# Optimization experiments

Hardware: AMD Instinct MI355X
Metric: run time of the kernel (lower is better)

Reference implementation:

```python
import jax, jax.numpy as jnp
import numpy as np
import math

N, LQ, C, HD, L, P = 2, 17821, 256, 8, 4, 4
D = C // HD
SHAPES = [(100, 134), (50, 67), (25, 34), (13, 17)]


def setup_inputs() -> dict:
    key = jax.random.key(0)
    ks = jax.random.split(key, 8)
    shapes = np.array(SHAPES, np.int32)
    areas = shapes[:, 0] * shapes[:, 1]
    starts = np.concatenate([[0], np.cumsum(areas)[:-1]]).astype(np.int32)
    Lin = int(areas.sum())
    sc = 1.0 / math.sqrt(C)
    # sampling_offsets bias: radial grid init as in _reset_parameters
    thetas = np.arange(HD, dtype=np.float32) * (2.0 * math.pi / HD)
    grid = np.stack([np.cos(thetas), np.sin(thetas)], -1)
    grid = grid / np.abs(grid).max(-1, keepdims=True)
    grid = np.tile(grid[:, None, None, :], (1, L, P, 1)) * np.arange(1, P + 1, dtype=np.float32)[None, None, :, None]
    boff = jnp.asarray(grid.reshape(-1), jnp.float32)
    return dict(
        query=jax.random.normal(ks[0], (N, LQ, C), jnp.float32),
        reference_points=jax.random.uniform(ks[1], (N, LQ, L, 2), jnp.float32),
        input_flatten=jax.random.normal(ks[2], (N, Lin, C), jnp.float32),
        input_spatial_shapes=jnp.asarray(shapes),
        input_level_start_index=jnp.asarray(starts),
        Wv=jax.random.normal(ks[3], (C, C), jnp.float32) * sc,
        bv=jnp.zeros((C,), jnp.float32),
        Woff=jax.random.normal(ks[4], (C, HD * L * P * 2), jnp.float32) * 0.01,
        boff=boff,
        Watt=jax.random.normal(ks[5], (C, HD * L * P), jnp.float32) * 0.02,
        batt=jnp.zeros((HD * L * P,), jnp.float32),
        Wout=jax.random.normal(ks[6], (C, C), jnp.float32) * sc,
        bout=jnp.zeros((C,), jnp.float32),
    )


def _ms_deform_attn_core(value, shapes, starts, loc, attw):
    # value: (N, Len_in, HD, D); loc: (N, Lq, HD, L, P, 2) in [0,1]; attw: (N, Lq, HD, L, P)
    n, lq = loc.shape[0], loc.shape[1]
    out = jnp.zeros((n, lq, HD, D), value.dtype)
    for l in range(L):
        H, W = int(shapes[l, 0]), int(shapes[l, 1])
        s = int(starts[l])
        v = value[:, s:s + H * W]                                    # (N, HW, HD, D)
        # (N,Lq,HD,P,2) -> (N,Lq,P,HD,2) -> (N,Lq*P,HD) per coord
        locl = loc[:, :, :, l].transpose(0, 1, 3, 2, 4).reshape(n, lq * P, HD, 2)
        # grid_sample align_corners=False mapping
        x = locl[..., 0] * W - 0.5
        y = locl[..., 1] * H - 0.5
        x0f, y0f = jnp.floor(x), jnp.floor(y)
        fx, fy = x - x0f, y - y0f
        x0, y0 = x0f.astype(jnp.int32), y0f.astype(jnp.int32)

        def corner(xi, yi, w):
            valid = (xi >= 0) & (xi < W) & (yi >= 0) & (yi < H)      # zero padding
            idx = jnp.clip(yi, 0, H - 1) * W + jnp.clip(xi, 0, W - 1)
            g = jnp.take_along_axis(v, idx[..., None], axis=1)        # (N, Lq*P, HD, D)
            return g * (w * valid)[..., None]

        samp = (corner(x0, y0, (1 - fx) * (1 - fy))
                + corner(x0 + 1, y0, fx * (1 - fy))
                + corner(x0, y0 + 1, (1 - fx) * fy)
                + corner(x0 + 1, y0 + 1, fx * fy))                    # (N, Lq*P, HD, D)
        aw = attw[:, :, :, l].transpose(0, 1, 3, 2).reshape(n, lq * P, HD)
        out = out + (samp * aw[..., None]).reshape(n, lq, P, HD, D).sum(axis=2)
    return out.reshape(n, lq, HD * D)


def reference(query, reference_points, input_flatten, input_spatial_shapes,
              input_level_start_index, Wv, bv, Woff, boff, Watt, batt, Wout, bout):
    shapes = np.asarray(input_spatial_shapes)
    starts = np.asarray(input_level_start_index)
    n, lq, _ = query.shape
    value = (input_flatten @ Wv + bv).reshape(n, -1, HD, D)
    offsets = (query @ Woff + boff).reshape(n, lq, HD, L, P, 2)
    # reference_points has last dim 2 -> normalize offsets by (W, H) per level
    norm = jnp.asarray(shapes[:, ::-1], jnp.float32)                  # (L, 2) = (W, H)
    loc = reference_points[:, :, None, :, None, :] + offsets / norm[None, None, None, :, None, :]
    attw = (query @ Watt + batt).reshape(n, lq, HD, L * P)
    attw = jax.nn.softmax(attw, axis=-1).reshape(n, lq, HD, L, P)
    out = _ms_deform_attn_core(value, shapes, starts, loc, attw)
    return out @ Wout + bout
```

## Files before the change

### kernel.cpp

```cpp
#include <hip/hip_runtime.h>
#include <hip/hip_bf16.h>
#include <math.h>

#define NB    2
#define LQ    17821
#define LIN   17821
#define CCH   256
#define HDN   8
#define DCH   32
#define LVL   4
#define NPT   4
#define KDIM  256

__constant__ const int   cH[LVL]  = {100, 50, 25, 13};
__constant__ const int   cW[LVL]  = {134, 67, 34, 17};
__constant__ const int   cS[LVL]  = {0, 13400, 16750, 17600};
__constant__ const float cHf[LVL] = {100.f, 50.f, 25.f, 13.f};
__constant__ const float cWf[LVL] = {134.f, 67.f, 34.f, 17.f};
__constant__ const float cRH[LVL] = {1.f/100.f, 1.f/50.f, 1.f/25.f, 1.f/13.f};
__constant__ const float cRW[LVL] = {1.f/134.f, 1.f/67.f, 1.f/34.f, 1.f/17.f};

typedef __attribute__((ext_vector_type(8))) _Float16 f16x8;
typedef __attribute__((ext_vector_type(4))) _Float16 f16x4;
typedef __attribute__((ext_vector_type(4))) float    f32x4;

__device__ __forceinline__ void glds16(const void* g, void* l) {
    __builtin_amdgcn_global_load_lds(
        (const __attribute__((address_space(1))) void*)g,
        (__attribute__((address_space(3))) void*)l, 16, 0, 0);
}

__global__ void prep_all(const float* __restrict__ Wv,
                         const float* __restrict__ Woff,
                         const float* __restrict__ Watt,
                         const float* __restrict__ Wout,
                         const float* __restrict__ boff,
                         const float* __restrict__ batt,
                         _Float16* __restrict__ wvT,
                         _Float16* __restrict__ wqT,
                         _Float16* __restrict__ wuT,
                         float* __restrict__ b384)
{
    const int i = blockIdx.x * 256 + threadIdx.x;
    if (i < 65536) {
        const int n = i >> 8, k = i & 255;
        wvT[i] = (_Float16)Wv[(size_t)k * 256 + n];
    } else if (i < 131072) {
        const int j = i - 65536, n = j >> 8, k = j & 255;
        wqT[j] = (_Float16)Woff[(size_t)k * 256 + n];
    } else if (i < 163840) {
        const int j = i - 131072, n = j >> 8, k = j & 255;
        wqT[65536 + j] = (_Float16)Watt[(size_t)k * 128 + n];
    } else if (i < 229376) {
        const int j = i - 163840, n = j >> 8, k = j & 255;
        wuT[j] = (_Float16)Wout[(size_t)k * 256 + n];
    } else {
        const int j = i - 229376;
        if (j < 256)      b384[j] = boff[j];
        else if (j < 384) b384[j] = batt[j - 256];
    }
}

__global__ void cvt_two(const float* __restrict__ X0, const float* __restrict__ X1,
                        _Float16* __restrict__ Y0, _Float16* __restrict__ Y1, int n4)
{
    const int stride = gridDim.x * 256;
    for (int i = blockIdx.x * 256 + threadIdx.x; i < 2 * n4; i += stride) {
        const bool second = i >= n4;
        const int j = second ? i - n4 : i;
        const float4 v = reinterpret_cast<const float4*>(second ? X1 : X0)[j];
        f16x4 h;
        h[0] = (_Float16)v.x; h[1] = (_Float16)v.y;
        h[2] = (_Float16)v.z; h[3] = (_Float16)v.w;
        reinterpret_cast<f16x4*>(second ? Y1 : Y0)[j] = h;
    }
}

template<typename OutT, bool PERM>
__global__ __launch_bounds__(256, 2) void gemm_tile(
    const _Float16* __restrict__ A,
    const _Float16* __restrict__ BT,
    const float* __restrict__ bias, OutT* __restrict__ C,
    int M, int Ntot)
{
    __shared__ _Float16 As[2][4096];
    __shared__ _Float16 Bs[2][4096];

    const int t    = threadIdx.x;
    const int wav  = t >> 6;
    const int lane = t & 63;
    const int bm   = blockIdx.y * 128;
    const int bn   = blockIdx.x * 128;

    const int wr = wav >> 1, wc = wav & 1;
    const int fcol = lane & 15;
    const int fk   = lane >> 4;

    int aoff[4], boff[4];
#pragma unroll
    for (int i = 0; i < 4; ++i) {
        const int ar = wr * 64 + i * 16 + fcol;
        aoff[i] = ar * 64 + ((fk ^ ((ar >> 1) & 3)) << 4);
        const int br = wc * 64 + i * 16 + fcol;
        boff[i] = br * 64 + ((fk ^ ((br >> 1) & 3)) << 4);
    }

    const int srow = lane >> 2;
    const int skb  = (lane & 3) << 4;

    f32x4 acc[4][4];
#pragma unroll
    for (int i = 0; i < 4; ++i)
#pragma unroll
        for (int j = 0; j < 4; ++j) acc[i][j] = (f32x4)(0.f);

    auto stage = [&](int s, int buf) {
        const int k0b = s * 64;
#pragma unroll
        for (int i = 0; i < 2; ++i) {
            const int j   = wav + i * 4;
            const int row = j * 16 + srow;
            const int kb  = skb ^ (((row >> 1) & 3) << 4);
            const int rga = min(bm + row, M - 1);
            glds16((const char*)A + (size_t)rga * 512 + k0b + kb,
                   (char*)As[buf] + j * 1024);
            const int rgb = bn + row;
            glds16((const char*)BT + (size_t)rgb * 512 + k0b + kb,
                   (char*)Bs[buf] + j * 1024);
        }
    };

    stage(0, 0);
    __syncthreads();
    int cur = 0;
#pragma unroll 1
    for (int s = 0; s < 8; ++s) {
        if (s + 1 < 8) stage(s + 1, cur ^ 1);
        f16x8 af[4], bfr[4];
#pragma unroll
        for (int i = 0; i < 4; ++i) {
            af[i]  = *reinterpret_cast<const f16x8*>((const char*)As[cur] + aoff[i]);
            bfr[i] = *reinterpret_cast<const f16x8*>((const char*)Bs[cur] + boff[i]);
        }
#pragma unroll
        for (int mi = 0; mi < 4; ++mi)
#pragma unroll
            for (int ni = 0; ni < 4; ++ni)
                acc[mi][ni] = __builtin_amdgcn_mfma_f32_16x16x32_f16(
                    af[mi], bfr[ni], acc[mi][ni], 0, 0, 0);
        __syncthreads();
        cur ^= 1;
    }

    const int r0 = bm + wr * 64 + (lane >> 4) * 4;
    const int c0 = bn + wc * 64 + fcol;
#pragma unroll
    for (int ni = 0; ni < 4; ++ni) {
        const int col = c0 + ni * 16;
        const float bv = bias[col];
#pragma unroll
        for (int mi = 0; mi < 4; ++mi) {
#pragma unroll
            for (int j = 0; j < 4; ++j) {
                const int r = r0 + mi * 16 + j;
                if (r < M) {
                    const float v = acc[mi][ni][j] + bv;
                    if (PERM) {
                        const int n   = (r >= LIN) ? 1 : 0;
                        const int pos = r - n * LIN;
                        const size_t dst = ((size_t)(n * HDN + (col >> 5)) * LIN + pos) * 32 + (col & 31);
                        C[dst] = (OutT)v;
                    } else {
                        C[(size_t)r * Ntot + col] = (OutT)v;
                    }
                }
            }
        }
    }
}

__global__ __launch_bounds__(256) void msda_sample(
    const _Float16* __restrict__ value,
    const _Float16* __restrict__ qproj,
    const float* __restrict__ refp,
    _Float16* __restrict__ o16)
{
    __shared__ int2 sIW[2][HDN][16][4];

    const int t = threadIdx.x;

    {
        const int qs = t >> 7;
        const int h  = (t >> 4) & 7;
        const int ip = t & 15;
        const int l  = ip >> 2;

        const int r = blockIdx.x * 2 + qs;
        const int n = r / LQ;
        const _Float16* qrow = qproj + (size_t)r * 384;

        const float logit = (float)qrow[256 + h * 16 + ip];
        float m = logit;
#pragma unroll
        for (int k = 8; k >= 1; k >>= 1) m = fmaxf(m, __shfl_xor(m, k));
        const float e = __expf(logit - m);
        float s = e;
#pragma unroll
        for (int k = 8; k >= 1; k >>= 1) s += __shfl_xor(s, k);
        const float aw = e / s;

        const float ox = (float)qrow[h * 32 + ip * 2 + 0];
        const float oy = (float)qrow[h * 32 + ip * 2 + 1];
        const float rx = refp[(size_t)r * 8 + l * 2 + 0];
        const float ry = refp[(size_t)r * 8 + l * 2 + 1];

        const int   Ww = cW[l], Hh = cH[l], st = cS[l];
        const float Wf = cWf[l], Hf = cHf[l];
        const float rW = cRW[l], rH = cRH[l];

        const float x = (rx + ox * rW) * Wf - 0.5f;
        const float y = (ry + oy * rH) * Hf - 0.5f;
        const float x0f = floorf(x);
        const float y0f = floorf(y);
        const float fx = x - x0f;
        const float fy = y - y0f;
        const int x0 = (int)x0f, y0 = (int)y0f;
        const int x1 = x0 + 1,   y1 = y0 + 1;

        const bool vx0 = (x0 >= 0) & (x0 < Ww);
        const bool vx1 = (x1 >= 0) & (x1 < Ww);
        const bool vy0 = (y0 >= 0) & (y0 < Hh);
        const bool vy1 = (y1 >= 0) & (y1 < Hh);

        const float gx0 = 1.f - fx, gx1 = fx;
        const float gy0 = 1.f - fy, gy1 = fy;

        const float w00 = (vx0 & vy0) ? gx0 * gy0 * aw : 0.f;
        const float w10 = (vx1 & vy0) ? gx1 * gy0 * aw : 0.f;
        const float w01 = (vx0 & vy1) ? gx0 * gy1 * aw : 0.f;
        const float w11 = (vx1 & vy1) ? gx1 * gy1 * aw : 0.f;

        const int xc0 = min(max(x0, 0), Ww - 1);
        const int xc1 = min(max(x1, 0), Ww - 1);
        const int yc0 = min(max(y0, 0), Hh - 1);
        const int yc1 = min(max(y1, 0), Hh - 1);

        const int base = (n * HDN + h) * LIN + st;
        sIW[qs][h][ip][0] = make_int2((base + yc0 * Ww + xc0) * 64, __float_as_int(w00));
        sIW[qs][h][ip][1] = make_int2((base + yc0 * Ww + xc1) * 64, __float_as_int(w10));
        sIW[qs][h][ip][2] = make_int2((base + yc1 * Ww + xc0) * 64, __float_as_int(w01));
        sIW[qs][h][ip][3] = make_int2((base + yc1 * Ww + xc1) * 64, __float_as_int(w11));
    }

    __syncthreads();

    const int g   = t >> 5;
    const int w   = t & 31;
    const int sub = w & 3;
    const int c   = (w >> 2) & 3;
    const int p2  = w >> 4;
    const char* vbase = (const char*)value + sub * 16;

    float acc0[8] = {}, acc1[8] = {};

#pragma unroll
    for (int i8 = 0; i8 < 8; ++i8) {
        const int ip = i8 * 2 + p2;
        const int2 iw0 = sIW[0][g][ip][c];
        const int2 iw1 = sIW[1][g][ip][c];
        const float wt0 = __int_as_float(iw0.y);
        const float wt1 = __int_as_float(iw1.y);
        const f16x8 v0 = *reinterpret_cast<const f16x8*>(vbase + iw0.x);
        const f16x8 v1 = *reinterpret_cast<const f16x8*>(vbase + iw1.x);
#pragma unroll
        for (int j = 0; j < 8; ++j) {
            acc0[j] = fmaf((float)v0[j], wt0, acc0[j]);
            acc1[j] = fmaf((float)v1[j], wt1, acc1[j]);
        }
    }

#pragma unroll
    for (int k = 4; k <= 16; k <<= 1) {
#pragma unroll
        for (int j = 0; j < 8; ++j) {
            acc0[j] += __shfl_xor(acc0[j], k);
            acc1[j] += __shfl_xor(acc1[j], k);
        }
    }

    if (w < 4) {
        const int r0 = blockIdx.x * 2;
        const size_t o = (size_t)r0 * 256 + g * 32 + sub * 8;
        f16x8 h0, h1;
#pragma unroll
        for (int j = 0; j < 8; ++j) {
            h0[j] = (_Float16)acc0[j];
            h1[j] = (_Float16)acc1[j];
        }
        *reinterpret_cast<f16x8*>(&o16[o])       = h0;
        *reinterpret_cast<f16x8*>(&o16[o + 256]) = h1;
    }
}

extern "C" void kernel_launch(void* const* d_in, const int* in_sizes, int n_in,
                              void* d_out, int out_size, void* d_ws, size_t ws_size,
                              hipStream_t stream)
{
    const float* query  = (const float*)d_in[0];
    const float* refp   = (const float*)d_in[1];
    const float* inflat = (const float*)d_in[2];
    const float* Wv     = (const float*)d_in[5];
    const float* bv     = (const float*)d_in[6];
    const float* Woff   = (const float*)d_in[7];
    const float* boff   = (const float*)d_in[8];
    const float* Watt   = (const float*)d_in[9];
    const float* batt   = (const float*)d_in[10];
    const float* Wout   = (const float*)d_in[11];
    const float* bout   = (const float*)d_in[12];
    float* out = (float*)d_out;

    const int M = NB * LQ;
    const size_t MC = (size_t)M * 256;

    float* ws   = (float*)d_ws;
    float* b384 = ws;

    _Float16* fbase = (_Float16*)(b384 + 384);
    _Float16* qp16  = fbase;
    _Float16* ih16  = qp16 + (size_t)M * 384;
    _Float16* qh16  = ih16 + MC;
    _Float16* v16   = qh16 + MC;
    _Float16* o16   = v16 + MC;
    _Float16* wvT   = o16 + MC;
    _Float16* wqT   = wvT + 65536;
    _Float16* wuT   = wqT + 98304;

    const dim3 blk(256);
    const int mblk = (M + 127) / 128;
    const int n4   = (int)(MC / 4);

    prep_all<<<dim3(898), blk, 0, stream>>>(Wv, Woff, Watt, Wout, boff, batt,
                                            wvT, wqT, wuT, b384);

    cvt_two<<<dim3(2048), blk, 0, stream>>>(inflat, query, ih16, qh16, n4);

    gemm_tile<_Float16, true><<<dim3(2, mblk), blk, 0, stream>>>(ih16, wvT, bv, v16, M, 256);
    gemm_tile<_Float16, false><<<dim3(3, mblk), blk, 0, stream>>>(qh16, wqT, b384, qp16, M, 384);

    msda_sample<<<dim3(M / 2), blk, 0, stream>>>(v16, qp16, refp, o16);

    gemm_tile<float, false><<<dim3(2, mblk), blk, 0, stream>>>(o16, wuT, bout, out, M, 256);
}
```

Baseline: 178.3 us.

## Fuse fp32-to-fp16 input conversion into GEMM staging and batch sampler gathers

Removes the separate conversion kernel and instead has the value and query GEMMs read fp32 activations directly, convert them in registers and write fp16 into swizzled shared memory. This avoids writing and re-reading two fp16 intermediate copies. The trade-off is that A-tile staging in those GEMMs becomes synchronous register loads instead of async global-to-LDS copies, which may expose latency. Separately, the sampling kernel now issues all 16 gather loads before doing any FMAs, to raise memory-level parallelism at the cost of more registers.

```diff
diff --git a/kernel.cpp b/kernel.cpp
--- a/kernel.cpp
+++ b/kernel.cpp
@@ -61,24 +61,9 @@
     }
 }
 
-__global__ void cvt_two(const float* __restrict__ X0, const float* __restrict__ X1,
-                        _Float16* __restrict__ Y0, _Float16* __restrict__ Y1, int n4)
-{
-    const int stride = gridDim.x * 256;
-    for (int i = blockIdx.x * 256 + threadIdx.x; i < 2 * n4; i += stride) {
-        const bool second = i >= n4;
-        const int j = second ? i - n4 : i;
-        const float4 v = reinterpret_cast<const float4*>(second ? X1 : X0)[j];
-        f16x4 h;
-        h[0] = (_Float16)v.x; h[1] = (_Float16)v.y;
-        h[2] = (_Float16)v.z; h[3] = (_Float16)v.w;
-        reinterpret_cast<f16x4*>(second ? Y1 : Y0)[j] = h;
-    }
-}
-
-template<typename OutT, bool PERM>
+template<typename AT, typename OutT, bool PERM>
 __global__ __launch_bounds__(256, 2) void gemm_tile(
-    const _Float16* __restrict__ A,
+    const AT* __restrict__ A,
     const _Float16* __restrict__ BT,
     const float* __restrict__ bias, OutT* __restrict__ C,
     int M, int Ntot)
@@ -106,7 +91,7 @@
     }
 
     const int srow = lane >> 2;
-    const int skb  = (lane & 3) << 4;
+    const int slot = lane & 3;
 
     f32x4 acc[4][4];
 #pragma unroll
@@ -115,18 +100,34 @@
         for (int j = 0; j < 4; ++j) acc[i][j] = (f32x4)(0.f);
 
     auto stage = [&](int s, int buf) {
-        const int k0b = s * 64;
 #pragma unroll
         for (int i = 0; i < 2; ++i) {
             const int j   = wav + i * 4;
             const int row = j * 16 + srow;
-            const int kb  = skb ^ (((row >> 1) & 3) << 4);
+            const int swz = ((row >> 1) & 3) << 4;
             const int rga = min(bm + row, M - 1);
-            glds16((const char*)A + (size_t)rga * 512 + k0b + kb,
-                   (char*)As[buf] + j * 1024);
-            const int rgb = bn + row;
-            glds16((const char*)BT + (size_t)rgb * 512 + k0b + kb,
-                   (char*)Bs[buf] + j * 1024);
+            if constexpr (sizeof(AT) == 2) {
+                const int kb = (slot << 4) ^ swz;
+                glds16((const char*)A + (size_t)rga * 512 + s * 64 + kb,
+                       (char*)As[buf] + j * 1024);
+            } else {
+                const char* src = (const char*)A + (size_t)rga * 1024 + s * 128 + slot * 32;
+                const float4 u0 = *reinterpret_cast<const float4*>(src);
+                const float4 u1 = *reinterpret_cast<const float4*>(src + 16);
+                f16x8 hv;
+                hv[0] = (_Float16)u0.x; hv[1] = (_Float16)u0.y;
+                hv[2] = (_Float16)u0.z; hv[3] = (_Float16)u0.w;
+                hv[4] = (_Float16)u1.x; hv[5] = (_Float16)u1.y;
+                hv[6] = (_Float16)u1.z; hv[7] = (_Float16)u1.w;
+                *reinterpret_cast<f16x8*>((char*)As[buf] + j * 1024 + srow * 64
+                                          + ((slot << 4) ^ swz)) = hv;
+            }
+            {
+                const int kb = (slot << 4) ^ swz;
+                const int rgb = bn + row;
+                glds16((const char*)BT + (size_t)rgb * 512 + s * 64 + kb,
+                       (char*)Bs[buf] + j * 1024);
+            }
         }
     };
 
@@ -261,21 +262,29 @@
     const int p2  = w >> 4;
     const char* vbase = (const char*)value + sub * 16;
 
+    int2 iwa[8], iwb[8];
+#pragma unroll
+    for (int i8 = 0; i8 < 8; ++i8) {
+        iwa[i8] = sIW[0][g][i8 * 2 + p2][c];
+        iwb[i8] = sIW[1][g][i8 * 2 + p2][c];
+    }
+
+    f16x8 va[8], vb[8];
+#pragma unroll
+    for (int i8 = 0; i8 < 8; ++i8) {
+        va[i8] = *reinterpret_cast<const f16x8*>(vbase + iwa[i8].x);
+        vb[i8] = *reinterpret_cast<const f16x8*>(vbase + iwb[i8].x);
+    }
+
     float acc0[8] = {}, acc1[8] = {};
-
 #pragma unroll
     for (int i8 = 0; i8 < 8; ++i8) {
-        const int ip = i8 * 2 + p2;
-        const int2 iw0 = sIW[0][g][ip][c];
-        const int2 iw1 = sIW[1][g][ip][c];
-        const float wt0 = __int_as_float(iw0.y);
-        const float wt1 = __int_as_float(iw1.y);
-        const f16x8 v0 = *reinterpret_cast<const f16x8*>(vbase + iw0.x);
-        const f16x8 v1 = *reinterpret_cast<const f16x8*>(vbase + iw1.x);
+        const float wt0 = __int_as_float(iwa[i8].y);
+        const float wt1 = __int_as_float(iwb[i8].y);
 #pragma unroll
         for (int j = 0; j < 8; ++j) {
-            acc0[j] = fmaf((float)v0[j], wt0, acc0[j]);
-            acc1[j] = fmaf((float)v1[j], wt1, acc1[j]);
+            acc0[j] = fmaf((float)va[i8][j], wt0, acc0[j]);
+            acc1[j] = fmaf((float)vb[i8][j], wt1, acc1[j]);
         }
     }
 
@@ -327,9 +336,7 @@
 
     _Float16* fbase = (_Float16*)(b384 + 384);
     _Float16* qp16  = fbase;
-    _Float16* ih16  = qp16 + (size_t)M * 384;
-    _Float16* qh16  = ih16 + MC;
-    _Float16* v16   = qh16 + MC;
+    _Float16* v16   = qp16 + (size_t)M * 384;
     _Float16* o16   = v16 + MC;
     _Float16* wvT   = o16 + MC;
     _Float16* wqT   = wvT + 65536;
@@ -337,17 +344,14 @@
 
     const dim3 blk(256);
     const int mblk = (M + 127) / 128;
-    const int n4   = (int)(MC / 4);
 
     prep_all<<<dim3(898), blk, 0, stream>>>(Wv, Woff, Watt, Wout, boff, batt,
                                             wvT, wqT, wuT, b384);
 
-    cvt_two<<<dim3(2048), blk, 0, stream>>>(inflat, query, ih16, qh16, n4);
-
-    gemm_tile<_Float16, true><<<dim3(2, mblk), blk, 0, stream>>>(ih16, wvT, bv, v16, M, 256);
-    gemm_tile<_Float16, false><<<dim3(3, mblk), blk, 0, stream>>>(qh16, wqT, b384, qp16, M, 384);
+    gemm_tile<float, _Float16, true><<<dim3(2, mblk), blk, 0, stream>>>(inflat, wvT, bv, v16, M, 256);
+    gemm_tile<float, _Float16, false><<<dim3(3, mblk), blk, 0, stream>>>(query, wqT, b384, qp16, M, 384);
 
     msda_sample<<<dim3(M / 2), blk, 0, stream>>>(v16, qp16, refp, o16);
 
-    gemm_tile<float, false><<<dim3(2, mblk), blk, 0, stream>>>(o16, wuT, bout, out, M, 256);
-}
+    gemm_tile<_Float16, float, false><<<dim3(2, mblk), blk, 0, stream>>>(o16, wuT, bout, out, M, 256);
+}
```

New measurement: 172.3 us. 1.03x faster.
